# Kernel tuning notes

Hardware: AMD Instinct MI355X
Metric: run time of the kernel (lower is better)

## Reference

```python
import jax, jax.numpy as jnp
import numpy as np

A = -0.75  # torch bicubic cubic-convolution coefficient

def _cubic_k(t):
    at = jnp.abs(t)
    return jnp.where(at <= 1, (A + 2) * at**3 - (A + 3) * at**2 + 1,
           jnp.where(at < 2, A * at**3 - 5 * A * at**2 + 8 * A * at - 4 * A, 0.0))

def _resize_last(x, out_size):
    # bicubic, align_corners=True, along last axis
    in_size = x.shape[-1]
    pos = jnp.arange(out_size, dtype=x.dtype) * ((in_size - 1) / (out_size - 1))
    i0 = jnp.floor(pos).astype(jnp.int32)
    frac = pos - i0
    offs = jnp.arange(-1, 3, dtype=jnp.int32)                    # 4 taps
    idx = jnp.clip(i0[None] + offs[:, None], 0, in_size - 1)     # [4, out]
    w = _cubic_k(frac[None] - offs[:, None].astype(x.dtype))     # [4, out]
    g = x[..., idx]                                              # [..., 4, out]
    return jnp.einsum('...ko,ko->...o', g, w)

def bicubic(x, H, W):
    x = _resize_last(x, W)
    x = jnp.swapaxes(_resize_last(jnp.swapaxes(x, -1, -2), H), -1, -2)
    return x

def conv(x, w, b):
    y = jax.lax.conv_general_dilated(x, w, (1, 1), 'SAME',
                                     dimension_numbers=('NCHW', 'OIHW', 'NCHW'))
    return y + b[None, :, None, None]

def pool(x):
    return jax.lax.reduce_window(x, -jnp.inf, jax.lax.max, (1, 1, 2, 2), (1, 1, 2, 2), 'VALID')

def extract(x, ws, bs):
    # feat1: vgg19 features[:2]
    x1 = jax.nn.relu(conv(x, ws[0], bs[0]))
    # feat2: vgg19 features[2:18]
    h = jax.nn.relu(conv(x1, ws[1], bs[1])); h = pool(h)
    h = jax.nn.relu(conv(h, ws[2], bs[2]))
    h = jax.nn.relu(conv(h, ws[3], bs[3])); h = pool(h)
    for i in range(4, 8):
        h = jax.nn.relu(conv(h, ws[i], bs[i]))
    h = bicubic(h, x1.shape[-2], x1.shape[-1])
    return jnp.concatenate([x1, h], axis=1)  # [B, 320, H, W]

def normalizer(f1, f2):
    B, C = f1.shape[:2]
    a = f1.reshape(B, C, -1)
    b = f2.reshape(B, C, -1)
    xc = jnp.concatenate([a, b], axis=-1)
    mean = xc.mean(-1, keepdims=True)
    std = xc.mean(-1, keepdims=True)  # faithful to original source bug: std = mean
    a = (a - mean) / (std + 1e-8)
    b = (b - mean) / (std + 1e-8)
    return a.reshape(f1.shape), b.reshape(f2.shape)

_CHANS = [(3, 64), (64, 64), (64, 128), (128, 128), (128, 256), (256, 256), (256, 256), (256, 256)]

def setup_inputs() -> dict:
    key = jax.random.key(0)
    ks = jax.random.split(key, 20)
    inp = {}
    for i, (ci, co) in enumerate(_CHANS):
        inp[f'w{i}'] = jax.random.normal(ks[i], (co, ci, 3, 3), jnp.float32) * np.sqrt(2.0 / (ci * 9))
        inp[f'b{i}'] = jnp.zeros((co,), jnp.float32)
    inp['x_ref'] = jax.random.normal(ks[16], (2, 3, 96, 96), jnp.float32)
    inp['x_template'] = jax.random.normal(ks[17], (2, 3, 48, 48), jnp.float32)
    inp['coef_ref'] = jnp.float32(1.0)
    inp['coef_tmp'] = jnp.float32(1.0)
    return inp

def reference(x_ref, x_template, coef_ref, coef_tmp,
              w0, b0, w1, b1, w2, b2, w3, b3, w4, b4, w5, b5, w6, b6, w7, b7):
    ws = [w0, w1, w2, w3, w4, w5, w6, w7]
    bs = [b0, b1, b2, b3, b4, b5, b6, b7]
    fref = extract(x_ref, ws, bs)
    ftem = extract(x_template, ws, bs)
    fref, ftem = normalizer(fref, ftem)
    B, C, m, n = fref.shape
    _, _, p, q = ftem.shape
    dist = jnp.einsum('bcmn,bcpq->bmnpq', fref, ftem).reshape(B, m * n, p * q)
    conf_ref = jax.nn.softmax(coef_ref * dist, axis=-2)
    conf_tmp = jax.nn.softmax(coef_tmp * dist, axis=-1)
    confidence = jnp.sqrt(conf_ref * conf_tmp)
    vals, _ = jax.lax.top_k(confidence, 10)
    values = vals.mean(-1, keepdims=True).reshape(B, m, n, 1)
    return values
```

## Files before the change

### kernel.cpp

```cpp
#include <hip/hip_runtime.h>
#include <math.h>

#define CK_A (-0.75f)

typedef __attribute__((ext_vector_type(8))) short bf16x8;
typedef __attribute__((ext_vector_type(4))) float f32x4;

struct CImg { const float* in; float* out; int H, W, tiles; long inBS, outBS, sStride; };

__device__ __forceinline__ float cubicw(float t){
  float at = fabsf(t);
  float at2 = at*at, at3 = at2*at;
  if (at <= 1.f) return (CK_A+2.f)*at3 - (CK_A+3.f)*at2 + 1.f;
  if (at < 2.f)  return CK_A*at3 - 5.f*CK_A*at2 + 8.f*CK_A*at - 4.f*CK_A;
  return 0.f;
}

__device__ __forceinline__ unsigned short f2bf_rne(float f){
  unsigned int u = __float_as_uint(f);
  unsigned int r = (u + 0x7fffu + ((u>>16)&1u)) >> 16;
  return (unsigned short)r;
}
__device__ __forceinline__ float bf2f(unsigned short h){
  return __uint_as_float(((unsigned int)h)<<16);
}

__device__ __forceinline__ void merge_ms(float& m, float& s, float m2, float s2){
  float M = fmaxf(m, m2);
  s = s*expf(m - M) + s2*expf(m2 - M);
  m = M;
}

#define MFB(a,b,c) __builtin_amdgcn_mfma_f32_16x16x32_bf16(a,b,c,0,0,0)

__global__ __launch_bounds__(256) void conv0_d(CImg A, CImg B,
    const float* __restrict__ w, const float* __restrict__ bias){
  bool isA = (int)blockIdx.x < A.tiles;
  const float* in = isA ? A.in : B.in;
  float* out = isA ? A.out : B.out;
  int H = isA ? A.H : B.H, W = isA ? A.W : B.W;
  long inBS = isA ? A.inBS : B.inBS, outBS = isA ? A.outBS : B.outBS;
  int tile = isA ? blockIdx.x : blockIdx.x - A.tiles;
  int tilesX = (W + 15) >> 4;
  int tx0 = (tile % tilesX) << 4, ty0 = (tile / tilesX) << 4;
  int cob = blockIdx.y * 4;
  int b = blockIdx.z;
  int lx = threadIdx.x & 15, ly = threadIdx.x >> 4;
  __shared__ float tile_s[3][18][20];
  float acc[4] = {0.f,0.f,0.f,0.f};
  const float* inb = in + (long)b*inBS;
  int ox = tx0+lx, oy = ty0+ly;

  for (int idx = threadIdx.x; idx < 3*324; idx += 256){
    int cl = idx/324, rem = idx - cl*324;
    int r = rem/18, c = rem - r*18;
    int gy = ty0 + r - 1, gx = tx0 + c - 1;
    const float* ic = inb + (long)cl*H*W;
    tile_s[cl][r][c] = (gy>=0 && gy<H && gx>=0 && gx<W) ? ic[(long)gy*W+gx] : 0.f;
  }
  __syncthreads();
  #pragma unroll
  for (int cl=0; cl<3; cl++){
    float t00=tile_s[cl][ly+0][lx+0], t01=tile_s[cl][ly+0][lx+1], t02=tile_s[cl][ly+0][lx+2];
    float t10=tile_s[cl][ly+1][lx+0], t11=tile_s[cl][ly+1][lx+1], t12=tile_s[cl][ly+1][lx+2];
    float t20=tile_s[cl][ly+2][lx+0], t21=tile_s[cl][ly+2][lx+1], t22=tile_s[cl][ly+2][lx+2];
    #pragma unroll
    for (int j=0;j<4;j++){
      const float* wp = w + ((long)(cob+j)*3 + cl)*9;
      float a = acc[j];
      a = fmaf(t00, wp[0], a); a = fmaf(t01, wp[1], a); a = fmaf(t02, wp[2], a);
      a = fmaf(t10, wp[3], a); a = fmaf(t11, wp[4], a); a = fmaf(t12, wp[5], a);
      a = fmaf(t20, wp[6], a); a = fmaf(t21, wp[7], a); a = fmaf(t22, wp[8], a);
      acc[j] = a;
    }
  }
  if (ox < W && oy < H){
    #pragma unroll
    for (int j=0;j<4;j++){
      float v = fmaxf(acc[j] + bias[cob+j], 0.f);
      out[(long)b*outBS + (long)(cob+j)*H*W + (long)oy*W + ox] = v;
    }
  }
}

__global__ void prep_w_all(const float* __restrict__ w1, const float* __restrict__ w2,
                           const float* __restrict__ w3, const float* __restrict__ w4,
                           const float* __restrict__ w5, const float* __restrict__ w6,
                           const float* __restrict__ w7, unsigned short* __restrict__ wp){
  const int ciT[7] = {64,64,128,128,256,256,256};
  const int coT[7] = {64,128,128,256,256,256,256};
  int l = blockIdx.y;
  const float* w = l==0?w1: l==1?w2: l==2?w3: l==3?w4: l==4?w5: l==5?w6: w7;
  long offv = 0;
  for (int i=0;i<7;i++){ if (i<l) offv += 9L*ciT[i]*coT[i]*2; }
  long total = 9L*ciT[l]*coT[l]*2;
  long e = (long)blockIdx.x*256 + threadIdx.x;
  if (e >= total) return;
  int CI = ciT[l], CO = coT[l];
  int j = (int)(e & 7);
  int lane = (int)((e>>3) & 63);
  int h = (int)((e>>9) & 1);
  long rem = e >> 10;
  int G = CO >> 4, KC = CI >> 5;
  int g = (int)(rem % G); long q = rem / G;
  int kc = (int)(q % KC); int o = (int)(q / KC);
  int co = (g<<4) + (lane & 15);
  int ci = (kc<<5) + ((lane>>4)<<3) + j;
  float v = w[((long)co*CI + ci)*9 + o];
  unsigned short hi = f2bf_rne(v);
  wp[offv + e] = (h==0) ? hi : f2bf_rne(v - bf2f(hi));
}

union AB { bf16x8 v; uint4 u; };

__global__ __launch_bounds__(256) void conv_mfma_d(
    CImg A, CImg B, const unsigned short* __restrict__ Wp,
    const float* __restrict__ bias, int CI, int CO, int nci, int S)
{
  bool isA = (int)blockIdx.x < A.tiles;
  const float* in = isA ? A.in : B.in;
  float* out = isA ? A.out : B.out;
  int H = isA ? A.H : B.H, W = isA ? A.W : B.W;
  long inBS = isA ? A.inBS : B.inBS, outBS = isA ? A.outBS : B.outBS;
  long sStride = isA ? A.sStride : B.sStride;
  int tile = isA ? blockIdx.x : blockIdx.x - A.tiles;

  int HW = H*W;
  int tilesX = (W+7)>>3;
  int tx0 = (tile % tilesX)<<3, ty0 = (tile / tilesX)<<3;
  int cobase = blockIdx.y << 6;
  int s = blockIdx.z % S, b = blockIdx.z / S;
  int tid = threadIdx.x, lane = tid & 63, wid = tid>>6;
  int wm = wid>>1, wn = wid&1;
  int KC = CI>>5, G = CO>>4;
  __shared__ __align__(16) unsigned short Bth[4000];
  __shared__ __align__(16) unsigned short Btl[4000];
  const float* inb = in + (long)b*inBS;

  int sofs[13]; int sla[13];
  #pragma unroll
  for (int i=0;i<13;i++){
    int e = tid + i*256;
    int cidx = e / 100, pix = e - cidx*100;
    int hy = pix/10, hx = pix - hy*10;
    int gy = ty0 - 1 + hy, gx = tx0 - 1 + hx;
    bool v = (gy>=0) && (gy<H) && (gx>=0) && (gx<W);
    sofs[i] = v ? (cidx*HW + gy*W + gx) : -1;
    sla[i] = pix*40 + cidx;
  }

  int n15 = lane & 15;
  int klane8 = (lane>>4)<<3;
  int p0 = wn*32 + n15;
  int base0 = ((p0>>3)*10 + (p0&7))*40 + klane8;
  int p1 = p0 + 16;
  int base1 = ((p1>>3)*10 + (p1&7))*40 + klane8;
  int g0 = (cobase>>4) + wm*2;

  f32x4 acc[2][2];
  #pragma unroll
  for (int i=0;i<2;i++)
    #pragma unroll
    for (int j=0;j<2;j++) acc[i][j] = (f32x4){0.f,0.f,0.f,0.f};

  int nkc = nci >> 5;
  for (int kk=0; kk<nkc; kk++){
    int ci0 = s*nci + (kk<<5);
    __syncthreads();
    #pragma unroll
    for (int i=0;i<12;i++){
      float v = (sofs[i] >= 0) ? inb[(long)ci0*HW + sofs[i]] : 0.f;
      unsigned short h = f2bf_rne(v);
      Bth[sla[i]] = h;
      Btl[sla[i]] = f2bf_rne(v - bf2f(h));
    }
    if (tid < 128){
      float v = (sofs[12] >= 0) ? inb[(long)ci0*HW + sofs[12]] : 0.f;
      unsigned short h = f2bf_rne(v);
      Bth[sla[12]] = h;
      Btl[sla[12]] = f2bf_rne(v - bf2f(h));
    }
    __syncthreads();
    int kc = ci0 >> 5;
    const unsigned short* wpb = Wp + (long)kc*G*1024 + (long)lane*8;
    #pragma unroll
    for (int o=0;o<9;o++){
      const int dy = o/3, dx = o - dy*3;
      const int sh = (dy*10+dx)*40;
      const unsigned short* wo = wpb + (long)o*KC*G*1024;
      AB a0h,a0l,a1h,a1l, b0h,b0l,b1h,b1l;
      a0h.u = *(const uint4*)(wo + (long)g0*1024);
      a0l.u = *(const uint4*)(wo + (long)g0*1024 + 512);
      a1h.u = *(const uint4*)(wo + (long)(g0+1)*1024);
      a1l.u = *(const uint4*)(wo + (long)(g0+1)*1024 + 512);
      b0h.v = *(const bf16x8*)&Bth[base0 + sh];
      b0l.v = *(const bf16x8*)&Btl[base0 + sh];
      b1h.v = *(const bf16x8*)&Bth[base1 + sh];
      b1l.v = *(const bf16x8*)&Btl[base1 + sh];
      acc[0][0] = MFB(a0h.v, b0l.v, acc[0][0]);
      acc[0][0] = MFB(a0l.v, b0h.v, acc[0][0]);
      acc[0][0] = MFB(a0h.v, b0h.v, acc[0][0]);
      acc[0][1] = MFB(a0h.v, b1l.v, acc[0][1]);
      acc[0][1] = MFB(a0l.v, b1h.v, acc[0][1]);
      acc[0][1] = MFB(a0h.v, b1h.v, acc[0][1]);
      acc[1][0] = MFB(a1h.v, b0l.v, acc[1][0]);
      acc[1][0] = MFB(a1l.v, b0h.v, acc[1][0]);
      acc[1][0] = MFB(a1h.v, b0h.v, acc[1][0]);
      acc[1][1] = MFB(a1h.v, b1l.v, acc[1][1]);
      acc[1][1] = MFB(a1l.v, b1h.v, acc[1][1]);
      acc[1][1] = MFB(a1h.v, b1h.v, acc[1][1]);
    }
  }

  float* outp = out + (long)s*sStride + (long)b*outBS;
  #pragma unroll
  for (int ng=0; ng<2; ng++){
    int p = wn*32 + ng*16 + n15;
    int gy = ty0 + (p>>3), gx = tx0 + (p&7);
    bool ok = (gy<H) && (gx<W);
    #pragma unroll
    for (int mg=0; mg<2; mg++){
      #pragma unroll
      for (int r=0;r<4;r++){
        if (ok){
          int co = cobase + wm*32 + mg*16 + ((lane>>4)<<2) + r;
          float v = acc[mg][ng][r];
          if (bias) v = fmaxf(v + bias[co], 0.f);
          outp[(long)co*HW + (long)gy*W + gx] = v;
        }
      }
    }
  }
}

__global__ void reduce_d(const float* __restrict__ pA, const float* __restrict__ pB,
                         const float* __restrict__ bias,
                         float* __restrict__ oA, float* __restrict__ oB,
                         int S, long sStrA, long sStrB, int CO, int HWa, int HWb,
                         long oBSa, long oBSb){
  int img = blockIdx.y;
  const float* part = img ? pB : pA;
  float* out = img ? oB : oA;
  int HW = img ? HWb : HWa;
  long sStride = img ? sStrB : sStrA;
  long outBS = img ? oBSb : oBSa;
  long tot = 2L*CO*HW;
  long e = (long)blockIdx.x*256 + threadIdx.x;
  if (e >= tot) return;
  long b = e / ((long)CO*HW);
  long r = e - b*(long)CO*HW;
  float v = 0.f;
  for (int s=0;s<S;s++) v += part[(long)s*sStride + e];
  int co = (int)(r / HW);
  out[b*outBS + r] = fmaxf(v + bias[co], 0.f);
}

__global__ void maxpool2_d(const float* __restrict__ inA, float* __restrict__ outA, long NCa, int HiA, int WiA,
                           const float* __restrict__ inB, float* __restrict__ outB, long NCb, int HiB, int WiB){
  const float* in = blockIdx.y ? inB : inA;
  float* out = blockIdx.y ? outB : outA;
  long NC = blockIdx.y ? NCb : NCa;
  int Hi = blockIdx.y ? HiB : HiA, Wi = blockIdx.y ? WiB : WiA;
  int Ho = Hi>>1, Wo = Wi>>1;
  long total = NC * Ho * Wo;
  long idx = (long)blockIdx.x*256 + threadIdx.x;
  if (idx >= total) return;
  int x = (int)(idx % Wo); long t = idx / Wo; int y = (int)(t % Ho); long nc = t / Ho;
  const float* p = in + (nc*Hi + 2*y)*(long)Wi + 2*x;
  out[idx] = fmaxf(fmaxf(p[0], p[1]), fmaxf(p[Wi], p[Wi+1]));
}

__global__ __launch_bounds__(256) void bicubic_d(
    const float* __restrict__ inA, float* __restrict__ outA,
    const float* __restrict__ inB, float* __restrict__ outB){
  int c = blockIdx.x;
  int img = blockIdx.y >> 1, b = blockIdx.y & 1;
  const float* in = img ? inB : inA;
  float* out = img ? outB : outA;
  int Hin = img ? 12 : 24, Win = Hin, Hout = img ? 48 : 96, Wout = Hout;
  long inBS = img ? 256L*144 : 256L*576;
  long outBS = img ? 320L*2304 : 320L*9216;
  __shared__ float s[576];
  const float* ip = in + (long)b*inBS + (long)c*Hin*Win;
  float* op = out + (long)b*outBS + (long)c*Hout*Wout;
  int n = Hin*Win;
  for (int i = threadIdx.x; i < n; i += 256) s[i] = ip[i];
  __syncthreads();
  float scy = (float)((double)(Hin-1)/(double)(Hout-1));
  float scx = scy;
  int total = Hout*Wout;
  for (int idx = threadIdx.x; idx < total; idx += 256){
    int ox = idx % Wout, oy = idx / Wout;
    float py = oy * scy, px = ox * scx;
    float iy0f = floorf(py), ix0f = floorf(px);
    int iy0 = (int)iy0f, ix0 = (int)ix0f;
    float fy = py - iy0f, fx = px - ix0f;
    float wy[4], wx[4]; int xs[4], ys[4];
    #pragma unroll
    for (int t=0;t<4;t++){
      wy[t] = cubicw(fy - (float)(t-1));
      wx[t] = cubicw(fx - (float)(t-1));
      ys[t] = min(max(iy0 + t - 1, 0), Hin-1);
      xs[t] = min(max(ix0 + t - 1, 0), Win-1);
    }
    float acc = 0.f;
    #pragma unroll
    for (int i=0;i<4;i++){
      const float* row = &s[ys[i]*Win];
      float rs = wx[0]*row[xs[0]] + wx[1]*row[xs[1]] + wx[2]*row[xs[2]] + wx[3]*row[xs[3]];
      acc = fmaf(wy[i], rs, acc);
    }
    op[idx] = acc;
  }
}

__global__ __launch_bounds__(256) void mean_k(const float* __restrict__ fR, const float* __restrict__ fT, float* __restrict__ mean){
  int c = blockIdx.x % 320, b = blockIdx.x / 320;
  const float* a = fR + ((long)b*320+c)*9216L;
  const float* t = fT + ((long)b*320+c)*2304L;
  float s = 0.f;
  for (int i=threadIdx.x;i<9216;i+=256) s += a[i];
  for (int i=threadIdx.x;i<2304;i+=256) s += t[i];
  __shared__ float sm[4];
  for (int o=32;o;o>>=1) s += __shfl_down(s,o);
  int lane = threadIdx.x & 63, wv = threadIdx.x >> 6;
  if (lane==0) sm[wv] = s;
  __syncthreads();
  if (threadIdx.x==0) mean[b*320+c] = (sm[0]+sm[1]+sm[2]+sm[3]) * (1.f/11520.f);
}

__global__ __launch_bounds__(256) void split_bf16(const float* __restrict__ feat,
    const float* __restrict__ mean,
    unsigned short* __restrict__ oh, unsigned short* __restrict__ ol, int P){
  int b = blockIdx.y; int m0 = blockIdx.x*32;
  __shared__ unsigned int t[32][321];
  int ml = threadIdx.x & 31, kq = threadIdx.x >> 5;
  const float* fp = feat + (long)b*320*P + m0 + ml;
  for (int k = kq*40; k < kq*40+40; k++){
    float mu = mean[b*320+k];
    float v = (fp[(long)k*P] - mu) / (mu + 1e-8f);
    unsigned short h = f2bf_rne(v);
    unsigned short l = f2bf_rne(v - bf2f(h));
    t[ml][k] = ((unsigned int)h<<16) | l;
  }
  __syncthreads();
  long base = ((long)b*P + m0)*320;
  for (int idx = threadIdx.x; idx < 32*320; idx += 256){
    int m = idx/320, k = idx - m*320;
    unsigned int p = t[m][k];
    oh[base + (long)m*320 + k] = (unsigned short)(p>>16);
    ol[base + (long)m*320 + k] = (unsigned short)(p & 0xffffu);
  }
}

union FragU { bf16x8 v; uint2 u[2]; };

__global__ __launch_bounds__(256) void gemm_mfma(
    const unsigned short* __restrict__ Ah, const unsigned short* __restrict__ Al,
    const unsigned short* __restrict__ Bh, const unsigned short* __restrict__ Bl,
    float* __restrict__ D, const float* __restrict__ coefr,
    float* __restrict__ pm, float* __restrict__ ps){
  const int N = 2304, K = 320;
  int n0 = blockIdx.x*128, m0 = blockIdx.y*128;
  __shared__ unsigned short As[2][128][36], Bs[2][128][36];
  int tid = threadIdx.x, lane = tid & 63, wid = tid >> 6;
  int wm = wid >> 1, wn = wid & 1;
  f32x4 acc[4][4];
  #pragma unroll
  for (int i=0;i<4;i++)
    #pragma unroll
    for (int j=0;j<4;j++) acc[i][j] = (f32x4){0.f,0.f,0.f,0.f};

  for (int k0=0; k0<K; k0+=32){
    #pragma unroll
    for (int q=0;q<2;q++){
      int flat = q*256 + tid;
      int row = flat >> 2, seg = flat & 3;
      long ga = (long)(m0+row)*K + k0 + seg*8;
      long gb = (long)(n0+row)*K + k0 + seg*8;
      uint4 va = *(const uint4*)(Ah + ga);
      *(uint2*)&As[0][row][seg*8]   = make_uint2(va.x, va.y);
      *(uint2*)&As[0][row][seg*8+4] = make_uint2(va.z, va.w);
      uint4 vb = *(const uint4*)(Al + ga);
      *(uint2*)&As[1][row][seg*8]   = make_uint2(vb.x, vb.y);
      *(uint2*)&As[1][row][seg*8+4] = make_uint2(vb.z, vb.w);
      uint4 vc = *(const uint4*)(Bh + gb);
      *(uint2*)&Bs[0][row][seg*8]   = make_uint2(vc.x, vc.y);
      *(uint2*)&Bs[0][row][seg*8+4] = make_uint2(vc.z, vc.w);
      uint4 vd = *(const uint4*)(Bl + gb);
      *(uint2*)&Bs[1][row][seg*8]   = make_uint2(vd.x, vd.y);
      *(uint2*)&Bs[1][row][seg*8+4] = make_uint2(vd.z, vd.w);
    }
    __syncthreads();

    FragU af[2][4], bf[2][4];
    #pragma unroll
    for (int g=0; g<4; g++){
      const unsigned short* pa0 = &As[0][wm*64 + g*16 + (lane&15)][(lane>>4)*4];
      const unsigned short* pa1 = &As[1][wm*64 + g*16 + (lane&15)][(lane>>4)*4];
      const unsigned short* pb0 = &Bs[0][wn*64 + g*16 + (lane&15)][(lane>>4)*4];
      const unsigned short* pb1 = &Bs[1][wn*64 + g*16 + (lane&15)][(lane>>4)*4];
      af[0][g].u[0] = *(const uint2*)pa0; af[0][g].u[1] = *(const uint2*)(pa0 + 16);
      af[1][g].u[0] = *(const uint2*)pa1; af[1][g].u[1] = *(const uint2*)(pa1 + 16);
      bf[0][g].u[0] = *(const uint2*)pb0; bf[0][g].u[1] = *(const uint2*)(pb0 + 16);
      bf[1][g].u[0] = *(const uint2*)pb1; bf[1][g].u[1] = *(const uint2*)(pb1 + 16);
    }
    #pragma unroll
    for (int mg=0; mg<4; mg++)
      #pragma unroll
      for (int ng=0; ng<4; ng++){
        acc[mg][ng] = MFB(af[0][mg].v, bf[1][ng].v, acc[mg][ng]);
        acc[mg][ng] = MFB(af[1][mg].v, bf[0][ng].v, acc[mg][ng]);
        acc[mg][ng] = MFB(af[0][mg].v, bf[0][ng].v, acc[mg][ng]);
      }
    __syncthreads();
  }

  #pragma unroll
  for (int mg=0; mg<4; mg++)
    #pragma unroll
    for (int ng=0; ng<4; ng++){
      int col = n0 + wn*64 + ng*16 + (lane & 15);
      #pragma unroll
      for (int r=0;r<4;r++){
        int rowv = m0 + wm*64 + mg*16 + (lane>>4)*4 + r;
        D[(long)rowv*N + col] = acc[mg][ng][r];
      }
    }

  float cr = *coefr;
  float* red = (float*)&As[0][0][0];
  float pmv[4], psv[4];
  #pragma unroll
  for (int ng=0; ng<4; ng++){
    float m = -INFINITY;
    #pragma unroll
    for (int mg=0; mg<4; mg++)
      #pragma unroll
      for (int r=0;r<4;r++) m = fmaxf(m, cr*acc[mg][ng][r]);
    float s = 0.f;
    #pragma unroll
    for (int mg=0; mg<4; mg++)
      #pragma unroll
      for (int r=0;r<4;r++) s += expf(cr*acc[mg][ng][r] - m);
    #pragma unroll
    for (int o=16;o<64;o<<=1){
      float m2 = __shfl_xor(m,o), s2 = __shfl_xor(s,o);
      merge_ms(m,s,m2,s2);
    }
    pmv[ng]=m; psv[ng]=s;
  }
  if ((lane>>4)==0){
    #pragma unroll
    for (int ng=0; ng<4; ng++){
      int cl = wn*64 + ng*16 + lane;
      red[wm*128 + cl] = pmv[ng];
      red[256 + wm*128 + cl] = psv[ng];
    }
  }
  __syncthreads();
  if (wm==0 && (lane>>4)==0){
    #pragma unroll
    for (int ng=0; ng<4; ng++){
      int cl = wn*64 + ng*16 + lane;
      float m = pmv[ng], s = psv[ng];
      merge_ms(m, s, red[128+cl], red[384+cl]);
      pm[(long)blockIdx.y*2304 + n0 + cl] = m;
      ps[(long)blockIdx.y*2304 + n0 + cl] = s;
    }
  }
}

__global__ void colstat_merge(const float* __restrict__ pm, const float* __restrict__ ps,
                              float* __restrict__ qcol){
  int idx = blockIdx.x*256 + threadIdx.x;
  if (idx >= 2304) return;
  float m=-INFINITY, s=0.f;
  for (int k=0;k<72;k++) merge_ms(m, s, pm[(long)k*2304+idx], ps[(long)k*2304+idx]);
  qcol[idx] = 0.5f*m + 0.5f*logf(s);
}

__global__ __launch_bounds__(256) void conf_topk_f(const float* __restrict__ D,
    const float* __restrict__ coefr, const float* __restrict__ coeft,
    const float* __restrict__ qcol, float* __restrict__ outp){
  int m = blockIdx.x;
  const float* drow = D + (long)m*2304;
  int tid = threadIdx.x, lane = tid & 63, wv = tid >> 6;
  float ct = *coeft, cr = *coefr;
  float v[9], tv[9];
  #pragma unroll
  for (int i=0;i<9;i++){ v[i] = drow[tid + i*256]; tv[i] = ct * v[i]; }

  __shared__ float sred[8];
  __shared__ unsigned int cand[40];

  float mx = tv[0];
  #pragma unroll
  for (int i=1;i<9;i++) mx = fmaxf(mx, tv[i]);
  #pragma unroll
  for (int o=1;o<64;o<<=1) mx = fmaxf(mx, __shfl_xor(mx, o));
  if (lane==0) sred[wv] = mx;
  __syncthreads();
  mx = fmaxf(fmaxf(sred[0],sred[1]), fmaxf(sred[2],sred[3]));
  float s = 0.f;
  #pragma unroll
  for (int i=0;i<9;i++) s += expf(tv[i]-mx);
  #pragma unroll
  for (int o=1;o<64;o<<=1) s += __shfl_xor(s, o);
  if (lane==0) sred[4+wv] = s;
  __syncthreads();
  float rs = sred[4]+sred[5]+sred[6]+sred[7];
  float rho = 0.5f*mx + 0.5f*logf(rs);
  float hc = 0.5f*(cr+ct);

  unsigned int key[9];
  #pragma unroll
  for (int i=0;i<9;i++){
    int n = i*256 + tid;
    float t = fmaf(hc, v[i], -qcol[n]);
    unsigned int b = __float_as_uint(t);
    b ^= (b >> 31) ? 0xFFFFFFFFu : 0x80000000u;
    key[i] = (b & 0xFFFFF000u) | (unsigned)n;
  }

  for (int t10=0; t10<10; t10++){
    unsigned int lb = key[0];
    #pragma unroll
    for (int i=1;i<9;i++) lb = lb > key[i] ? lb : key[i];
    unsigned int wb = lb;
    #pragma unroll
    for (int o=1;o<64;o<<=1){
      unsigned int x = (unsigned int)__shfl_xor((int)wb, o);
      wb = wb > x ? wb : x;
    }
    if (lane==0) cand[wv*10 + t10] = wb;
    #pragma unroll
    for (int i=0;i<9;i++) if (key[i]==wb) key[i]=0;
  }
  __syncthreads();

  if (wv == 0){
    unsigned int k = (lane < 40) ? cand[lane] : 0u;
    int sel = -1;
    for (int t10=0; t10<10; t10++){
      unsigned int wb = k;
      #pragma unroll
      for (int o=1;o<64;o<<=1){
        unsigned int x = (unsigned int)__shfl_xor((int)wb, o);
        wb = wb > x ? wb : x;
      }
      if (k == wb) k = 0;
      if (lane == t10) sel = (int)(wb & 0xFFFu);
    }
    float c = 0.f;
    if (sel >= 0){
      float t = fmaf(hc, drow[sel], -qcol[sel]);
      c = expf(t - rho);
    }
    #pragma unroll
    for (int o=1;o<64;o<<=1) c += __shfl_xor(c, o);
    if (lane == 0) outp[m] = c * 0.1f;
  }
}

extern "C" void kernel_launch(void* const* d_in, const int* in_sizes, int n_in,
                              void* d_out, int out_size, void* d_ws, size_t ws_size,
                              hipStream_t stream) {
  const float *W[8], *Bp[8], *xr, *xt, *cr, *ct;
  if (in_sizes[0] == 1728){
    for (int i=0;i<8;i++){ W[i]=(const float*)d_in[2*i]; Bp[i]=(const float*)d_in[2*i+1]; }
    xr=(const float*)d_in[16]; xt=(const float*)d_in[17];
    cr=(const float*)d_in[18]; ct=(const float*)d_in[19];
  } else {
    xr=(const float*)d_in[0]; xt=(const float*)d_in[1];
    cr=(const float*)d_in[2]; ct=(const float*)d_in[3];
    for (int i=0;i<8;i++){ W[i]=(const float*)d_in[4+2*i]; Bp[i]=(const float*)d_in[5+2*i]; }
  }

  const int convCI[8] = {3,64,64,128,128,256,256,256};
  const int convCO[8] = {64,64,128,128,256,256,256,256};
  long wpoff[8]; long wtot = 0;
  for (int l=1;l<8;l++){ wpoff[l] = wtot; wtot += 9L*convCI[l]*convCO[l]*2; }

  float* ws = (float*)d_ws;
  long off = 0;
  auto alloc = [&](long nfl){ float* p = ws + off; off += (nfl + 63) & ~63L; return p; };
  float* featR = alloc(2L*320*9216);
  float* featT = alloc(2L*320*2304);
  float* meanb = alloc(640);
  float* pm    = alloc(72L*2304);
  float* ps    = alloc(72L*2304);
  float* qcol  = alloc(2304);
  unsigned short* wp = (unsigned short*)alloc((wtot+1)/2);
  float* scratch = alloc(9216L*2304);
  if ((size_t)(off*4) > ws_size) return;

  unsigned short* AhR = (unsigned short*)alloc((2L*9216*320 + 1)/2);
  unsigned short* AlR = (unsigned short*)alloc((2L*9216*320 + 1)/2);
  unsigned short* BhT = (unsigned short*)alloc((2L*2304*320 + 1)/2);
  unsigned short* BlT = (unsigned short*)alloc((2L*2304*320 + 1)/2);
  if ((size_t)(off*4) > ws_size) return;

  float* rA = scratch;
  float* rB = rA + 1179648;
  float* rC = rB + 294912;
  float* rD = rC + 589824;
  float* rE = rD + 589824;
  float* rF = rE + 147456;
  float* rG = rF + 294912;
  float* a2 = rG + 294912;
  float* b2 = a2 + 294912;
  float* c2 = b2 + 73728;
  float* d2 = c2 + 147456;
  float* e2 = d2 + 147456;
  float* f2 = e2 + 36864;
  float* g2 = f2 + 73728;
  float* tPR = g2 + 73728;
  float* tPT = tPR + 1179648;
  float* dist = scratch;

  auto mkimg = [](const float* in, float* out, int H, int Wd, int tiles,
                  long inBS, long outBS, long sStr){
    CImg c; c.in=in; c.out=out; c.H=H; c.W=Wd; c.tiles=tiles;
    c.inBS=inBS; c.outBS=outBS; c.sStride=sStr; return c;
  };

  prep_w_all<<<dim3(4608,7), 256, 0, stream>>>(W[1],W[2],W[3],W[4],W[5],W[6],W[7], wp);

  {
    CImg A = mkimg(xr, featR, 96,96, 36, 3L*9216, 320L*9216, 0);
    CImg B = mkimg(xt, featT, 48,48, 9, 3L*2304, 320L*2304, 0);
    conv0_d<<<dim3(45,16,2), 256, 0, stream>>>(A, B, W[0], Bp[0]);
  }
  {
    CImg A = mkimg(featR, rA, 96,96, 144, 320L*9216, 64L*9216, 0);
    CImg B = mkimg(featT, a2, 48,48, 36, 320L*2304, 64L*2304, 0);
    conv_mfma_d<<<dim3(180,1,2), 256, 0, stream>>>(A,B, wp+wpoff[1], Bp[1], 64,64,64,1);
  }
  maxpool2_d<<<dim3(1152,2), 256, 0, stream>>>(rA,rB,128,96,96, a2,b2,128,48,48);
  {
    CImg A = mkimg(rB, tPR, 48,48, 36, 64L*2304, 128L*2304, 589824);
    CImg B = mkimg(b2, tPT, 24,24, 9, 64L*576, 128L*576, 147456);
    conv_mfma_d<<<dim3(45,2,4), 256, 0, stream>>>(A,B, wp+wpoff[2], nullptr, 64,128,32,2);
    reduce_d<<<dim3(2304,2), 256, 0, stream>>>(tPR,tPT,Bp[2], rC,c2, 2, 589824,147456, 128, 2304,576, 128L*2304, 128L*576);
  }
  {
    CImg A = mkimg(rC, tPR, 48,48, 36, 128L*2304, 128L*2304, 589824);
    CImg B = mkimg(c2, tPT, 24,24, 9, 128L*576, 128L*576, 147456);
    conv_mfma_d<<<dim3(45,2,4), 256, 0, stream>>>(A,B, wp+wpoff[3], nullptr, 128,128,64,2);
    reduce_d<<<dim3(2304,2), 256, 0, stream>>>(tPR,tPT,Bp[3], rD,d2, 2, 589824,147456, 128, 2304,576, 128L*2304, 128L*576);
  }
  maxpool2_d<<<dim3(576,2), 256, 0, stream>>>(rD,rE,256,48,48, d2,e2,256,24,24);
  {
    CImg A = mkimg(rE, tPR, 24,24, 9, 128L*576, 256L*576, 294912);
    CImg B = mkimg(e2, tPT, 12,12, 4, 128L*144, 256L*144, 73728);
    conv_mfma_d<<<dim3(13,4,8), 256, 0, stream>>>(A,B, wp+wpoff[4], nullptr, 128,256,32,4);
    reduce_d<<<dim3(1152,2), 256, 0, stream>>>(tPR,tPT,Bp[4], rF,f2, 4, 294912,73728, 256, 576,144, 256L*576, 256L*144);
  }
  const float* inR[3] = {rF, rG, rF};  float* outR[3] = {rG, rF, rG};
  const float* inT[3] = {f2, g2, f2};  float* outT[3] = {g2, f2, g2};
  for (int i=0;i<3;i++){
    int l = 5+i;
    CImg A = mkimg(inR[i], tPR, 24,24, 9, 256L*576, 256L*576, 294912);
    CImg B = mkimg(inT[i], tPT, 12,12, 4, 256L*144, 256L*144, 73728);
    conv_mfma_d<<<dim3(13,4,8), 256, 0, stream>>>(A,B, wp+wpoff[l], nullptr, 256,256,64,4);
    reduce_d<<<dim3(1152,2), 256, 0, stream>>>(tPR,tPT,Bp[l], outR[i],outT[i], 4, 294912,73728, 256, 576,144, 256L*576, 256L*144);
  }
  bicubic_d<<<dim3(256,4), 256, 0, stream>>>(rG, featR + 64L*9216, g2, featT + 64L*2304);

  mean_k<<<640, 256, 0, stream>>>(featR, featT, meanb);
  split_bf16<<<dim3(288,2), 256, 0, stream>>>(featR, meanb, AhR, AlR, 9216);
  split_bf16<<<dim3(72,2),  256, 0, stream>>>(featT, meanb, BhT, BlT, 2304);

  for (int b=0; b<2; b++){
    gemm_mfma<<<dim3(18,72), 256, 0, stream>>>(
        AhR + (long)b*9216*320, AlR + (long)b*9216*320,
        BhT + (long)b*2304*320, BlT + (long)b*2304*320, dist, cr, pm, ps);
    colstat_merge<<<dim3(9), 256, 0, stream>>>(pm, ps, qcol);
    conf_topk_f<<<dim3(9216), 256, 0, stream>>>(dist, cr, ct, qcol, (float*)d_out + (long)b*9216);
  }
}
```

Baseline: 499.9 us.

## Fuse split-K partial reduction, bias and ReLU into consumer kernel loads

Removes the separate reduce_d kernels. Each consumer (next conv's input staging, maxpool, bicubic) now sums the split-K partials, adds bias and applies ReLU on load. Split counts rise for several conv layers to give more parallelism, the two split_bf16 launches merge into one, and precise expf/logf become __expf/__logf. The cost is repeated partial summation across tiles and taps, which reads more data per element, plus lower accuracy from the fast exp/log intrinsics.

Measured after the change: 627.8 us. +25.6%, slower.

```diff
diff --git a/kernel.cpp b/kernel.cpp
--- a/kernel.cpp
+++ b/kernel.cpp
@@ -27,7 +27,7 @@
 
 __device__ __forceinline__ void merge_ms(float& m, float& s, float m2, float s2){
   float M = fmaxf(m, m2);
-  s = s*expf(m - M) + s2*expf(m2 - M);
+  s = s*__expf(m - M) + s2*__expf(m2 - M);
   m = M;
 }
 
@@ -115,7 +115,9 @@
 
 __global__ __launch_bounds__(256) void conv_mfma_d(
     CImg A, CImg B, const unsigned short* __restrict__ Wp,
-    const float* __restrict__ bias, int CI, int CO, int nci, int S)
+    const float* __restrict__ bias, const float* __restrict__ biasIn,
+    int SIN, long sInStrA, long sInStrB,
+    int CI, int CO, int nci, int S)
 {
   bool isA = (int)blockIdx.x < A.tiles;
   const float* in = isA ? A.in : B.in;
@@ -123,6 +125,7 @@
   int H = isA ? A.H : B.H, W = isA ? A.W : B.W;
   long inBS = isA ? A.inBS : B.inBS, outBS = isA ? A.outBS : B.outBS;
   long sStride = isA ? A.sStride : B.sStride;
+  long sInStr = isA ? sInStrA : sInStrB;
   int tile = isA ? blockIdx.x : blockIdx.x - A.tiles;
 
   int HW = H*W;
@@ -137,7 +140,7 @@
   __shared__ __align__(16) unsigned short Btl[4000];
   const float* inb = in + (long)b*inBS;
 
-  int sofs[13]; int sla[13];
+  int sofs[13]; int sla[13]; int scix[13];
   #pragma unroll
   for (int i=0;i<13;i++){
     int e = tid + i*256;
@@ -147,6 +150,7 @@
     bool v = (gy>=0) && (gy<H) && (gx>=0) && (gx<W);
     sofs[i] = v ? (cidx*HW + gy*W + gx) : -1;
     sla[i] = pix*40 + cidx;
+    scix[i] = cidx;
   }
 
   int n15 = lane & 15;
@@ -168,17 +172,21 @@
     int ci0 = s*nci + (kk<<5);
     __syncthreads();
     #pragma unroll
-    for (int i=0;i<12;i++){
-      float v = (sofs[i] >= 0) ? inb[(long)ci0*HW + sofs[i]] : 0.f;
+    for (int i=0;i<13;i++){
+      if (i==12 && tid >= 128) break;
+      float v = 0.f;
+      if (sofs[i] >= 0){
+        long ga = (long)ci0*HW + sofs[i];
+        if (SIN == 0) v = inb[ga];
+        else {
+          float a = biasIn[ci0 + scix[i]];
+          for (int s2=0; s2<SIN; s2++) a += inb[(long)s2*sInStr + ga];
+          v = fmaxf(a, 0.f);
+        }
+      }
       unsigned short h = f2bf_rne(v);
       Bth[sla[i]] = h;
       Btl[sla[i]] = f2bf_rne(v - bf2f(h));
-    }
-    if (tid < 128){
-      float v = (sofs[12] >= 0) ? inb[(long)ci0*HW + sofs[12]] : 0.f;
-      unsigned short h = f2bf_rne(v);
-      Bth[sla[12]] = h;
-      Btl[sla[12]] = f2bf_rne(v - bf2f(h));
     }
     __syncthreads();
     int kc = ci0 >> 5;
@@ -233,50 +241,46 @@
   }
 }
 
-__global__ void reduce_d(const float* __restrict__ pA, const float* __restrict__ pB,
-                         const float* __restrict__ bias,
-                         float* __restrict__ oA, float* __restrict__ oB,
-                         int S, long sStrA, long sStrB, int CO, int HWa, int HWb,
-                         long oBSa, long oBSb){
-  int img = blockIdx.y;
-  const float* part = img ? pB : pA;
-  float* out = img ? oB : oA;
-  int HW = img ? HWb : HWa;
-  long sStride = img ? sStrB : sStrA;
-  long outBS = img ? oBSb : oBSa;
-  long tot = 2L*CO*HW;
-  long e = (long)blockIdx.x*256 + threadIdx.x;
-  if (e >= tot) return;
-  long b = e / ((long)CO*HW);
-  long r = e - b*(long)CO*HW;
-  float v = 0.f;
-  for (int s=0;s<S;s++) v += part[(long)s*sStride + e];
-  int co = (int)(r / HW);
-  out[b*outBS + r] = fmaxf(v + bias[co], 0.f);
-}
-
 __global__ void maxpool2_d(const float* __restrict__ inA, float* __restrict__ outA, long NCa, int HiA, int WiA,
-                           const float* __restrict__ inB, float* __restrict__ outB, long NCb, int HiB, int WiB){
+                           const float* __restrict__ inB, float* __restrict__ outB, long NCb, int HiB, int WiB,
+                           const float* __restrict__ biasIn, int SIN, long sStrA, long sStrB, int CO){
   const float* in = blockIdx.y ? inB : inA;
   float* out = blockIdx.y ? outB : outA;
   long NC = blockIdx.y ? NCb : NCa;
+  long sStr = blockIdx.y ? sStrB : sStrA;
   int Hi = blockIdx.y ? HiB : HiA, Wi = blockIdx.y ? WiB : WiA;
   int Ho = Hi>>1, Wo = Wi>>1;
   long total = NC * Ho * Wo;
   long idx = (long)blockIdx.x*256 + threadIdx.x;
   if (idx >= total) return;
   int x = (int)(idx % Wo); long t = idx / Wo; int y = (int)(t % Ho); long nc = t / Ho;
-  const float* p = in + (nc*Hi + 2*y)*(long)Wi + 2*x;
-  out[idx] = fmaxf(fmaxf(p[0], p[1]), fmaxf(p[Wi], p[Wi+1]));
+  long pbase = nc*(long)Hi*Wi + (long)(2*y)*Wi + 2*x;
+  if (SIN == 0){
+    const float* p = in + pbase;
+    out[idx] = fmaxf(fmaxf(p[0], p[1]), fmaxf(p[Wi], p[Wi+1]));
+  } else {
+    float bI = biasIn[(int)(nc % CO)];
+    long po[4] = {pbase, pbase+1, pbase+Wi, pbase+Wi+1};
+    float mx = -INFINITY;
+    #pragma unroll
+    for (int k=0;k<4;k++){
+      float a = bI;
+      for (int s=0;s<SIN;s++) a += in[(long)s*sStr + po[k]];
+      mx = fmaxf(mx, fmaxf(a, 0.f));
+    }
+    out[idx] = mx;
+  }
 }
 
 __global__ __launch_bounds__(256) void bicubic_d(
     const float* __restrict__ inA, float* __restrict__ outA,
-    const float* __restrict__ inB, float* __restrict__ outB){
+    const float* __restrict__ inB, float* __restrict__ outB,
+    const float* __restrict__ biasIn, int SIN, long sStrA, long sStrB){
   int c = blockIdx.x;
   int img = blockIdx.y >> 1, b = blockIdx.y & 1;
   const float* in = img ? inB : inA;
   float* out = img ? outB : outA;
+  long sStr = img ? sStrB : sStrA;
   int Hin = img ? 12 : 24, Win = Hin, Hout = img ? 48 : 96, Wout = Hout;
   long inBS = img ? 256L*144 : 256L*576;
   long outBS = img ? 320L*2304 : 320L*9216;
@@ -284,7 +288,12 @@
   const float* ip = in + (long)b*inBS + (long)c*Hin*Win;
   float* op = out + (long)b*outBS + (long)c*Hout*Wout;
   int n = Hin*Win;
-  for (int i = threadIdx.x; i < n; i += 256) s[i] = ip[i];
+  float bI = biasIn[c];
+  for (int i = threadIdx.x; i < n; i += 256){
+    float a = bI;
+    for (int s2=0;s2<SIN;s2++) a += ip[(long)s2*sStr + i];
+    s[i] = fmaxf(a, 0.f);
+  }
   __syncthreads();
   float scy = (float)((double)(Hin-1)/(double)(Hout-1));
   float scx = scy;
@@ -329,10 +338,17 @@
   if (threadIdx.x==0) mean[b*320+c] = (sm[0]+sm[1]+sm[2]+sm[3]) * (1.f/11520.f);
 }
 
-__global__ __launch_bounds__(256) void split_bf16(const float* __restrict__ feat,
+__global__ __launch_bounds__(256) void split_bf16_d(const float* __restrict__ fR, const float* __restrict__ fT,
     const float* __restrict__ mean,
-    unsigned short* __restrict__ oh, unsigned short* __restrict__ ol, int P){
-  int b = blockIdx.y; int m0 = blockIdx.x*32;
+    unsigned short* __restrict__ AhR, unsigned short* __restrict__ AlR,
+    unsigned short* __restrict__ BhT, unsigned short* __restrict__ BlT){
+  bool isR = blockIdx.x < 288;
+  const float* feat = isR ? fR : fT;
+  unsigned short* oh = isR ? AhR : BhT;
+  unsigned short* ol = isR ? AlR : BlT;
+  int P = isR ? 9216 : 2304;
+  int m0 = (isR ? blockIdx.x : blockIdx.x - 288) * 32;
+  int b = blockIdx.y;
   __shared__ unsigned int t[32][321];
   int ml = threadIdx.x & 31, kq = threadIdx.x >> 5;
   const float* fp = feat + (long)b*320*P + m0 + ml;
@@ -442,7 +458,7 @@
     #pragma unroll
     for (int mg=0; mg<4; mg++)
       #pragma unroll
-      for (int r=0;r<4;r++) s += expf(cr*acc[mg][ng][r] - m);
+      for (int r=0;r<4;r++) s += __expf(cr*acc[mg][ng][r] - m);
     #pragma unroll
     for (int o=16;o<64;o<<=1){
       float m2 = __shfl_xor(m,o), s2 = __shfl_xor(s,o);
@@ -477,7 +493,7 @@
   if (idx >= 2304) return;
   float m=-INFINITY, s=0.f;
   for (int k=0;k<72;k++) merge_ms(m, s, pm[(long)k*2304+idx], ps[(long)k*2304+idx]);
-  qcol[idx] = 0.5f*m + 0.5f*logf(s);
+  qcol[idx] = 0.5f*m + 0.5f*__logf(s);
 }
 
 __global__ __launch_bounds__(256) void conf_topk_f(const float* __restrict__ D,
@@ -504,13 +520,13 @@
   mx = fmaxf(fmaxf(sred[0],sred[1]), fmaxf(sred[2],sred[3]));
   float s = 0.f;
   #pragma unroll
-  for (int i=0;i<9;i++) s += expf(tv[i]-mx);
+  for (int i=0;i<9;i++) s += __expf(tv[i]-mx);
   #pragma unroll
   for (int o=1;o<64;o<<=1) s += __shfl_xor(s, o);
   if (lane==0) sred[4+wv] = s;
   __syncthreads();
   float rs = sred[4]+sred[5]+sred[6]+sred[7];
-  float rho = 0.5f*mx + 0.5f*logf(rs);
+  float rho = 0.5f*mx + 0.5f*__logf(rs);
   float hc = 0.5f*(cr+ct);
 
   unsigned int key[9];
@@ -555,7 +571,7 @@
     float c = 0.f;
     if (sel >= 0){
       float t = fmaf(hc, drow[sel], -qcol[sel]);
-      c = expf(t - rho);
+      c = __expf(t - rho);
     }
     #pragma unroll
     for (int o=1;o<64;o<<=1) c += __shfl_xor(c, o);
@@ -601,22 +617,16 @@
   unsigned short* BlT = (unsigned short*)alloc((2L*2304*320 + 1)/2);
   if ((size_t)(off*4) > ws_size) return;
 
-  float* rA = scratch;
-  float* rB = rA + 1179648;
-  float* rC = rB + 294912;
-  float* rD = rC + 589824;
-  float* rE = rD + 589824;
-  float* rF = rE + 147456;
-  float* rG = rF + 294912;
-  float* a2 = rG + 294912;
-  float* b2 = a2 + 294912;
-  float* c2 = b2 + 73728;
-  float* d2 = c2 + 147456;
-  float* e2 = d2 + 147456;
-  float* f2 = e2 + 36864;
-  float* g2 = f2 + 73728;
-  float* tPR = g2 + 73728;
-  float* tPT = tPR + 1179648;
+  float* rA  = scratch;
+  float* rB  = rA  + 1179648;
+  float* a2  = rB  + 294912;
+  float* b2  = a2  + 294912;
+  float* rE  = b2  + 73728;
+  float* e2  = rE  + 147456;
+  float* PR1 = e2  + 36864;
+  float* PR2 = PR1 + 2359296;
+  float* PT1 = PR2 + 2359296;
+  float* PT2 = PT1 + 589824;
   float* dist = scratch;
 
   auto mkimg = [](const float* in, float* out, int H, int Wd, int tiles,
@@ -635,42 +645,45 @@
   {
     CImg A = mkimg(featR, rA, 96,96, 144, 320L*9216, 64L*9216, 0);
     CImg B = mkimg(featT, a2, 48,48, 36, 320L*2304, 64L*2304, 0);
-    conv_mfma_d<<<dim3(180,1,2), 256, 0, stream>>>(A,B, wp+wpoff[1], Bp[1], 64,64,64,1);
-  }
-  maxpool2_d<<<dim3(1152,2), 256, 0, stream>>>(rA,rB,128,96,96, a2,b2,128,48,48);
-  {
-    CImg A = mkimg(rB, tPR, 48,48, 36, 64L*2304, 128L*2304, 589824);
-    CImg B = mkimg(b2, tPT, 24,24, 9, 64L*576, 128L*576, 147456);
-    conv_mfma_d<<<dim3(45,2,4), 256, 0, stream>>>(A,B, wp+wpoff[2], nullptr, 64,128,32,2);
-    reduce_d<<<dim3(2304,2), 256, 0, stream>>>(tPR,tPT,Bp[2], rC,c2, 2, 589824,147456, 128, 2304,576, 128L*2304, 128L*576);
-  }
-  {
-    CImg A = mkimg(rC, tPR, 48,48, 36, 128L*2304, 128L*2304, 589824);
-    CImg B = mkimg(c2, tPT, 24,24, 9, 128L*576, 128L*576, 147456);
-    conv_mfma_d<<<dim3(45,2,4), 256, 0, stream>>>(A,B, wp+wpoff[3], nullptr, 128,128,64,2);
-    reduce_d<<<dim3(2304,2), 256, 0, stream>>>(tPR,tPT,Bp[3], rD,d2, 2, 589824,147456, 128, 2304,576, 128L*2304, 128L*576);
-  }
-  maxpool2_d<<<dim3(576,2), 256, 0, stream>>>(rD,rE,256,48,48, d2,e2,256,24,24);
-  {
-    CImg A = mkimg(rE, tPR, 24,24, 9, 128L*576, 256L*576, 294912);
-    CImg B = mkimg(e2, tPT, 12,12, 4, 128L*144, 256L*144, 73728);
-    conv_mfma_d<<<dim3(13,4,8), 256, 0, stream>>>(A,B, wp+wpoff[4], nullptr, 128,256,32,4);
-    reduce_d<<<dim3(1152,2), 256, 0, stream>>>(tPR,tPT,Bp[4], rF,f2, 4, 294912,73728, 256, 576,144, 256L*576, 256L*144);
-  }
-  const float* inR[3] = {rF, rG, rF};  float* outR[3] = {rG, rF, rG};
-  const float* inT[3] = {f2, g2, f2};  float* outT[3] = {g2, f2, g2};
-  for (int i=0;i<3;i++){
-    int l = 5+i;
-    CImg A = mkimg(inR[i], tPR, 24,24, 9, 256L*576, 256L*576, 294912);
-    CImg B = mkimg(inT[i], tPT, 12,12, 4, 256L*144, 256L*144, 73728);
-    conv_mfma_d<<<dim3(13,4,8), 256, 0, stream>>>(A,B, wp+wpoff[l], nullptr, 256,256,64,4);
-    reduce_d<<<dim3(1152,2), 256, 0, stream>>>(tPR,tPT,Bp[l], outR[i],outT[i], 4, 294912,73728, 256, 576,144, 256L*576, 256L*144);
-  }
-  bicubic_d<<<dim3(256,4), 256, 0, stream>>>(rG, featR + 64L*9216, g2, featT + 64L*2304);
+    conv_mfma_d<<<dim3(180,1,2), 256, 0, stream>>>(A,B, wp+wpoff[1], Bp[1], nullptr,0,0,0, 64,64,64,1);
+  }
+  maxpool2_d<<<dim3(1152,2), 256, 0, stream>>>(rA,rB,128,96,96, a2,b2,128,48,48, nullptr,0,0,0,64);
+  {
+    CImg A = mkimg(rB, PR1, 48,48, 36, 64L*2304, 128L*2304, 589824);
+    CImg B = mkimg(b2, PT1, 24,24, 9, 64L*576, 128L*576, 147456);
+    conv_mfma_d<<<dim3(45,2,4), 256, 0, stream>>>(A,B, wp+wpoff[2], nullptr, nullptr,0,0,0, 64,128,32,2);
+  }
+  {
+    CImg A = mkimg(PR1, PR2, 48,48, 36, 128L*2304, 128L*2304, 589824);
+    CImg B = mkimg(PT1, PT2, 24,24, 9, 128L*576, 128L*576, 147456);
+    conv_mfma_d<<<dim3(45,2,8), 256, 0, stream>>>(A,B, wp+wpoff[3], nullptr, Bp[2],2,589824,147456, 128,128,32,4);
+  }
+  maxpool2_d<<<dim3(576,2), 256, 0, stream>>>(PR2,rE,256,48,48, PT2,e2,256,24,24, Bp[3],4,589824,147456,128);
+  {
+    CImg A = mkimg(rE, PR1, 24,24, 9, 128L*576, 256L*576, 294912);
+    CImg B = mkimg(e2, PT1, 12,12, 4, 128L*144, 256L*144, 73728);
+    conv_mfma_d<<<dim3(13,4,8), 256, 0, stream>>>(A,B, wp+wpoff[4], nullptr, nullptr,0,0,0, 128,256,32,4);
+  }
+  {
+    CImg A = mkimg(PR1, PR2, 24,24, 9, 256L*576, 256L*576, 294912);
+    CImg B = mkimg(PT1, PT2, 12,12, 4, 256L*144, 256L*144, 73728);
+    conv_mfma_d<<<dim3(13,4,16), 256, 0, stream>>>(A,B, wp+wpoff[5], nullptr, Bp[4],4,294912,73728, 256,256,32,8);
+  }
+  {
+    CImg A = mkimg(PR2, PR1, 24,24, 9, 256L*576, 256L*576, 294912);
+    CImg B = mkimg(PT2, PT1, 12,12, 4, 256L*144, 256L*144, 73728);
+    conv_mfma_d<<<dim3(13,4,16), 256, 0, stream>>>(A,B, wp+wpoff[6], nullptr, Bp[5],8,294912,73728, 256,256,32,8);
+  }
+  {
+    CImg A = mkimg(PR1, PR2, 24,24, 9, 256L*576, 256L*576, 294912);
+    CImg B = mkimg(PT1, PT2, 12,12, 4, 256L*144, 256L*144, 73728);
+    conv_mfma_d<<<dim3(13,4,16), 256, 0, stream>>>(A,B, wp+wpoff[7], nullptr, Bp[6],8,294912,73728, 256,256,32,8);
+  }
+  bicubic_d<<<dim3(256,4), 256, 0, stream>>>(PR2, featR + 64L*9216, PT2, featT + 64L*2304,
+                                             Bp[7], 8, 294912, 73728);
 
   mean_k<<<640, 256, 0, stream>>>(featR, featT, meanb);
-  split_bf16<<<dim3(288,2), 256, 0, stream>>>(featR, meanb, AhR, AlR, 9216);
-  split_bf16<<<dim3(72,2),  256, 0, stream>>>(featT, meanb, BhT, BlT, 2304);
+  split_bf16_d<<<dim3(360,2), 256, 0, stream>>>(featR, featT, meanb, AhR, AlR, BhT, BlT);
 
   for (int b=0; b<2; b++){
     gemm_mfma<<<dim3(18,72), 256, 0, stream>>>(
```
